# Kernel tuning notes

Hardware: AMD Instinct MI355X
Metric: run time of the kernel (lower is better)

Reference implementation:

```python
import jax, jax.numpy as jnp
import numpy as np

N, C, T, H, W = 4, 512, 8, 28, 28
CQ, CV = C // 8, C // 2  # 64, 256


def _maxpool222(a):
    # max_pool3d with kernel=stride=(2,2,2), VALID, over (t,h,w) of [n,c,t,h,w]
    return jax.lax.reduce_window(a, -jnp.inf, jax.lax.max,
                                 (1, 1, 2, 2, 2), (1, 1, 2, 2, 2), 'VALID')


def setup_inputs() -> dict:
    key = jax.random.key(0)
    ks = jax.random.split(key, 6)
    s = lambda fan_in: 1.0 / np.sqrt(fan_in)
    return {
        'x':  jax.random.normal(ks[0], (N, C, T, H, W), dtype=jnp.float32),
        'Wq': jax.random.normal(ks[1], (CQ, C), dtype=jnp.float32) * s(C),
        'Wk': jax.random.normal(ks[2], (CQ, C), dtype=jnp.float32) * s(C),
        'Wv': jax.random.normal(ks[3], (CV, C), dtype=jnp.float32) * s(C),
        'Wz': jax.random.normal(ks[4], (C, CV), dtype=jnp.float32) * s(CV),
        'y':  jax.random.normal(ks[5], (), dtype=jnp.float32) * 0.1,
    }


def reference(x, Wq, Wk, Wv, Wz, y):
    n, c, t, h, w = x.shape
    # 1x1x1 convs (no bias) = per-voxel channel mixing
    q = jnp.einsum('ncthw,oc->nothw', x, Wq)          # [n, CQ, t, h, w]
    k = _maxpool222(jnp.einsum('ncthw,oc->nothw', x, Wk))  # [n, CQ, t/2, h/2, w/2]
    v = _maxpool222(jnp.einsum('ncthw,oc->nothw', x, Wv))  # [n, CV, t/2, h/2, w/2]

    Lq = t * h * w
    Lk = k.shape[2] * k.shape[3] * k.shape[4]
    qf = q.reshape(n, q.shape[1], Lq)                 # [n, CQ, Lq]
    kf = k.reshape(n, k.shape[1], Lk)                 # [n, CQ, Lk]
    vf = v.reshape(n, v.shape[1], Lk)                 # [n, CV, Lk]

    # beta = softmax(q^T k) over kv axis (NOTE: no 1/sqrt(d) scaling, as in source)
    beta = jax.nn.softmax(jnp.einsum('ncq,nck->nqk', qf, kf), axis=-1)  # [n, Lq, Lk]
    att = jnp.einsum('nck,nqk->ncq', vf, beta)        # [n, CV, Lq]
    att = att.reshape(n, vf.shape[1], t, h, w)

    z = jnp.einsum('ncthw,oc->nothw', att, Wz)        # [n, C, t, h, w]
    return y * z + x
```

## Files before the change

### kernel.cpp

```cpp
#include <hip/hip_runtime.h>
#include <hip/hip_bf16.h>

#define LSP  6272
#define LK   784
#define CIN  512
#define CQo  64
#define CVo  256
#define NB   4

typedef __bf16  bf16x8 __attribute__((ext_vector_type(8)));
typedef __bf16  bf16x4 __attribute__((ext_vector_type(4)));
typedef float   f32x4  __attribute__((ext_vector_type(4)));

#define LDT  40

__global__ __launch_bounds__(256) void xt_kernel(const float* __restrict__ x,
                                                 __bf16* __restrict__ xT)
{
    __shared__ __attribute__((aligned(16))) __bf16 tile[64][68];
    int t = threadIdx.x;
    int p0 = blockIdx.x * 64, c0 = blockIdx.y * 64, n = blockIdx.z;
    #pragma unroll
    for (int i = 0; i < 4; i++) {
        int idx = i * 256 + t;
        int c = idx >> 4, p4 = (idx & 15) * 4;
        const float4 v = *reinterpret_cast<const float4*>(
            &x[((size_t)(n * CIN + c0 + c)) * LSP + p0 + p4]);
        tile[p4 + 0][c] = (__bf16)v.x;
        tile[p4 + 1][c] = (__bf16)v.y;
        tile[p4 + 2][c] = (__bf16)v.z;
        tile[p4 + 3][c] = (__bf16)v.w;
    }
    __syncthreads();
    #pragma unroll
    for (int i = 0; i < 4; i++) {
        int idx = i * 256 + t;
        int p = idx >> 4, c4 = (idx & 15) * 4;
        bf16x4 o;
        o[0] = tile[p][c4 + 0]; o[1] = tile[p][c4 + 1];
        o[2] = tile[p][c4 + 2]; o[3] = tile[p][c4 + 3];
        *reinterpret_cast<bf16x4*>(&xT[((size_t)(n * LSP + p0 + p)) * CIN + c0 + c4]) = o;
    }
}

__global__ void wprep_kernel(const float* __restrict__ Wq, const float* __restrict__ Wk,
                             const float* __restrict__ Wv, const float* __restrict__ Wz,
                             __bf16* __restrict__ Wqkv, __bf16* __restrict__ Wzb)
{
    int idx = blockIdx.x * 256 + threadIdx.x;
    if (idx < 384 * 512) {
        int o = idx >> 9;
        float v = (o < 64) ? Wq[idx] : (o < 128) ? Wk[idx - 64 * 512] : Wv[idx - 128 * 512];
        Wqkv[idx] = (__bf16)v;
    }
    if (idx < 512 * 256) Wzb[idx] = (__bf16)Wz[idx];
}

__global__ __launch_bounds__(256) void qkv_gemm(const __bf16* __restrict__ Wqkv,
                                                const __bf16* __restrict__ xT,
                                                __bf16* __restrict__ qT,
                                                __bf16* __restrict__ kT,
                                                __bf16* __restrict__ vconv)
{
    __shared__ __attribute__((aligned(16))) __bf16 As[2][128 * LDT];
    __shared__ __attribute__((aligned(16))) __bf16 Bs[2][128 * LDT];
    int t = threadIdx.x;
    int p0 = blockIdx.x * 128;
    int m0 = blockIdx.y * 128;
    int n  = blockIdx.z;
    int lane = t & 63, wid = t >> 6;
    int wm = wid >> 1, wn = wid & 1;
    int lm = lane & 15, lk = lane >> 4;

    const __bf16* wsrc = &Wqkv[(size_t)(m0 + (t >> 2)) * CIN + (t & 3) * 8];
    const __bf16* xsrc = &xT[((size_t)(n * LSP + p0 + (t >> 2))) * CIN + (t & 3) * 8];
    int dsoff = (t >> 2) * LDT + (t & 3) * 8;

    uint4 wa[2], xb[2];
    f32x4 acc[4][4] = {};

    wa[0] = *reinterpret_cast<const uint4*>(wsrc);
    wa[1] = *reinterpret_cast<const uint4*>(wsrc + 64 * CIN);
    xb[0] = *reinterpret_cast<const uint4*>(xsrc);
    xb[1] = *reinterpret_cast<const uint4*>(xsrc + 64 * CIN);
    *reinterpret_cast<uint4*>(&As[0][dsoff]) = wa[0];
    *reinterpret_cast<uint4*>(&As[0][dsoff + 64 * LDT]) = wa[1];
    *reinterpret_cast<uint4*>(&Bs[0][dsoff]) = xb[0];
    *reinterpret_cast<uint4*>(&Bs[0][dsoff + 64 * LDT]) = xb[1];
    __syncthreads();

    for (int kt = 0; kt < 16; kt++) {
        int cur = kt & 1;
        if (kt < 15) {
            int ko = (kt + 1) * 32;
            wa[0] = *reinterpret_cast<const uint4*>(wsrc + ko);
            wa[1] = *reinterpret_cast<const uint4*>(wsrc + 64 * CIN + ko);
            xb[0] = *reinterpret_cast<const uint4*>(xsrc + ko);
            xb[1] = *reinterpret_cast<const uint4*>(xsrc + 64 * CIN + ko);
        }
        bf16x8 a[4], b[4];
        if (m0 == 0) {
            #pragma unroll
            for (int mi = 0; mi < 4; mi++)
                a[mi] = *reinterpret_cast<const bf16x8*>(&As[cur][(wm * 64 + mi * 16 + lm) * LDT + lk * 8]);
            #pragma unroll
            for (int ni = 0; ni < 4; ni++)
                b[ni] = *reinterpret_cast<const bf16x8*>(&Bs[cur][(wn * 64 + ni * 16 + lm) * LDT + lk * 8]);
        } else {
            #pragma unroll
            for (int mi = 0; mi < 4; mi++)
                a[mi] = *reinterpret_cast<const bf16x8*>(&Bs[cur][(wn * 64 + mi * 16 + lm) * LDT + lk * 8]);
            #pragma unroll
            for (int ni = 0; ni < 4; ni++)
                b[ni] = *reinterpret_cast<const bf16x8*>(&As[cur][(wm * 64 + ni * 16 + lm) * LDT + lk * 8]);
        }
        #pragma unroll
        for (int mi = 0; mi < 4; mi++)
            #pragma unroll
            for (int ni = 0; ni < 4; ni++)
                acc[mi][ni] = __builtin_amdgcn_mfma_f32_16x16x32_bf16(a[mi], b[ni], acc[mi][ni], 0, 0, 0);
        if (kt < 15) {
            *reinterpret_cast<uint4*>(&As[cur ^ 1][dsoff]) = wa[0];
            *reinterpret_cast<uint4*>(&As[cur ^ 1][dsoff + 64 * LDT]) = wa[1];
            *reinterpret_cast<uint4*>(&Bs[cur ^ 1][dsoff]) = xb[0];
            *reinterpret_cast<uint4*>(&Bs[cur ^ 1][dsoff + 64 * LDT]) = xb[1];
        }
        __syncthreads();
    }

    if (m0 == 0) {
        #pragma unroll
        for (int mi = 0; mi < 4; mi++) {
            int mloc = wm * 64 + mi * 16 + lk * 4;
            #pragma unroll
            for (int ni = 0; ni < 4; ni++) {
                int p = p0 + wn * 64 + ni * 16 + lm;
                bf16x4 o;
                o[0] = (__bf16)acc[mi][ni][0]; o[1] = (__bf16)acc[mi][ni][1];
                o[2] = (__bf16)acc[mi][ni][2]; o[3] = (__bf16)acc[mi][ni][3];
                if (mloc < 64)
                    *reinterpret_cast<bf16x4*>(&qT[((size_t)(n * LSP + p)) * 64 + mloc]) = o;
                else
                    *reinterpret_cast<bf16x4*>(&kT[((size_t)(n * LSP + p)) * 64 + (mloc - 64)]) = o;
            }
        }
    } else {
        #pragma unroll
        for (int mi = 0; mi < 4; mi++) {
            int p = p0 + wn * 64 + mi * 16 + lk * 4;
            #pragma unroll
            for (int ni = 0; ni < 4; ni++) {
                int cv = (m0 - 128) + wm * 64 + ni * 16 + lm;
                bf16x4 o;
                o[0] = (__bf16)acc[mi][ni][0]; o[1] = (__bf16)acc[mi][ni][1];
                o[2] = (__bf16)acc[mi][ni][2]; o[3] = (__bf16)acc[mi][ni][3];
                *reinterpret_cast<bf16x4*>(&vconv[((size_t)(n * CVo + cv)) * LSP + p]) = o;
            }
        }
    }
}

__global__ __launch_bounds__(256) void poolk_kernel(const __bf16* __restrict__ kT,
                                                    __bf16* __restrict__ kpT)
{
    int wid = threadIdx.x >> 6, lane = threadIdx.x & 63;
    int row = blockIdx.x * 4 + wid;
    int n = row / LK, pk = row % LK;
    int tp = pk / 196, rem = pk % 196, hp = rem / 14, wp = rem % 14;
    const __bf16* b = kT + ((size_t)n * LSP + tp * 2 * 784 + hp * 2 * 28 + wp * 2) * 64 + lane;
    float m =        (float)b[0];
    m = fmaxf(m, (float)b[64]);
    m = fmaxf(m, (float)b[28 * 64]);
    m = fmaxf(m, (float)b[29 * 64]);
    m = fmaxf(m, (float)b[784 * 64]);
    m = fmaxf(m, (float)b[785 * 64]);
    m = fmaxf(m, (float)b[812 * 64]);
    m = fmaxf(m, (float)b[813 * 64]);
    kpT[(size_t)row * 64 + lane] = (__bf16)m;
}

__global__ void poolv_kernel(const __bf16* __restrict__ vconv, __bf16* __restrict__ vp)
{
    int id = blockIdx.x * 256 + threadIdx.x;
    if (id >= NB * CVo * LK) return;
    int nc = id / LK, pk = id % LK;
    int tp = pk / 196, rem = pk % 196, hp = rem / 14, wp = rem % 14;
    const __bf16* b = vconv + (size_t)nc * LSP + tp * 2 * 784 + hp * 2 * 28 + wp * 2;
    float m =        (float)b[0];
    m = fmaxf(m, (float)b[1]);   m = fmaxf(m, (float)b[28]);  m = fmaxf(m, (float)b[29]);
    m = fmaxf(m, (float)b[784]); m = fmaxf(m, (float)b[785]); m = fmaxf(m, (float)b[812]); m = fmaxf(m, (float)b[813]);
    vp[id] = (__bf16)m;
}

__global__ __launch_bounds__(512) void flash3_kernel(
    const __bf16* __restrict__ qT, const __bf16* __restrict__ kpT,
    const __bf16* __restrict__ vp, __bf16* __restrict__ attT)
{
    __shared__ __attribute__((aligned(16))) __bf16 Kbuf[2][64 * 64];
    __shared__ __attribute__((aligned(16))) __bf16 Ps[128 * 64];
    __shared__ float scs[128];
    __shared__ float invl[128];

    int t = threadIdx.x;
    int lane = t & 63, w = t >> 6;
    int lm = lane & 15, lk = lane >> 4;
    int q0 = blockIdx.x * 128;
    int n  = blockIdx.y;
    int swz = (lm & 7) << 3;

    const __bf16* kbase = kpT + (size_t)n * LK * 64;
    const __bf16* vbase = vp  + (size_t)n * CVo * LK;

    bf16x8 qa[2];
    {
        const __bf16* qrow = &qT[((size_t)(n * LSP + q0 + w * 16 + lm)) * 64 + lk * 8];
        qa[0] = *reinterpret_cast<const bf16x8*>(qrow);
        qa[1] = *reinterpret_cast<const bf16x8*>(qrow + 32);
    }

    int kr = t >> 3, kc = t & 7;
    int kds = kr * 64 + ((kc * 8) ^ ((kr & 7) << 3));
    const __bf16* kgsrc = &kbase[(size_t)kr * 64 + kc * 8];

    const __bf16* vsrc[2][2];
    #pragma unroll
    for (int mi = 0; mi < 2; mi++)
        #pragma unroll
        for (int ks = 0; ks < 2; ks++)
            vsrc[mi][ks] = &vbase[(size_t)(w * 32 + mi * 16 + lm) * LK + ks * 32 + lk * 8];

    uint4 kreg;
    bf16x8 vcur[2][2], vnxt[2][2];

    kreg = *reinterpret_cast<const uint4*>(kgsrc);
    #pragma unroll
    for (int mi = 0; mi < 2; mi++)
        #pragma unroll
        for (int ks = 0; ks < 2; ks++)
            vcur[mi][ks] = *reinterpret_cast<const bf16x8*>(vsrc[mi][ks]);
    *reinterpret_cast<uint4*>(&Kbuf[0][kds]) = kreg;
    __syncthreads();

    f32x4 accO[2][8] = {};
    float m = -1e30f, l = 0.0f;
    int qrow = w * 16 + lm;

    for (int kt = 0; kt < 13; kt++) {
        int cur = kt & 1;
        bool have_next = (kt < 12);
        bool lastT = (kt == 12);
        if (have_next) {
            size_t off = (size_t)(kt + 1) * 64;
            kreg = *reinterpret_cast<const uint4*>(kgsrc + off * 64);
            #pragma unroll
            for (int mi = 0; mi < 2; mi++)
                #pragma unroll
                for (int ks = 0; ks < 2; ks++)
                    vnxt[mi][ks] = *reinterpret_cast<const bf16x8*>(vsrc[mi][ks] + off);
        }
        f32x4 accS[4] = {};
        #pragma unroll
        for (int kg = 0; kg < 4; kg++) {
            if (!lastT || kg == 0) {
                #pragma unroll
                for (int ks = 0; ks < 2; ks++) {
                    bf16x8 kf = *reinterpret_cast<const bf16x8*>(
                        &Kbuf[cur][(kg * 16 + lm) * 64 + ((ks * 32 + lk * 8) ^ swz)]);
                    accS[kg] = __builtin_amdgcn_mfma_f32_16x16x32_bf16(kf, qa[ks], accS[kg], 0, 0, 0);
                }
            } else {
                accS[kg][0] = -1e30f; accS[kg][1] = -1e30f;
                accS[kg][2] = -1e30f; accS[kg][3] = -1e30f;
            }
        }
        float v = -1e30f;
        #pragma unroll
        for (int kg = 0; kg < 4; kg++)
            #pragma unroll
            for (int r = 0; r < 4; r++) v = fmaxf(v, accS[kg][r]);
        v = fmaxf(v, __shfl_xor(v, 16));
        v = fmaxf(v, __shfl_xor(v, 32));
        float sc_out = 1.0f;
        if (__any(v - m > 8.0f)) {
            float mn = fmaxf(m, v);
            sc_out = __expf(m - mn);
            l *= sc_out;
            m = mn;
        }
        float lt = 0.0f;
        #pragma unroll
        for (int kg = 0; kg < 4; kg++) {
            bf16x4 pw;
            #pragma unroll
            for (int r = 0; r < 4; r++) {
                float p = __expf(accS[kg][r] - m);
                lt += p;
                pw[r] = (__bf16)p;
            }
            *reinterpret_cast<bf16x4*>(&Ps[qrow * 64 + ((kg * 16 + lk * 4) ^ swz)]) = pw;
        }
        lt += __shfl_xor(lt, 16);
        lt += __shfl_xor(lt, 32);
        l += lt;
        if (lk == 0) scs[qrow] = sc_out;
        __syncthreads();
        float s[8];
        #pragma unroll
        for (int ni = 0; ni < 8; ni++) s[ni] = scs[ni * 16 + lm];
        bool need = false;
        #pragma unroll
        for (int ni = 0; ni < 8; ni++) need = need || (s[ni] != 1.0f);
        if (__any(need)) {
            #pragma unroll
            for (int mi = 0; mi < 2; mi++)
                #pragma unroll
                for (int ni = 0; ni < 8; ni++)
                    #pragma unroll
                    for (int r = 0; r < 4; r++) accO[mi][ni][r] *= s[ni];
        }
        #pragma unroll
        for (int ks = 0; ks < 2; ks++) {
            bf16x8 pf[8];
            #pragma unroll
            for (int ni = 0; ni < 8; ni++)
                pf[ni] = *reinterpret_cast<const bf16x8*>(
                    &Ps[(ni * 16 + lm) * 64 + ((ks * 32 + lk * 8) ^ swz)]);
            #pragma unroll
            for (int mi = 0; mi < 2; mi++)
                #pragma unroll
                for (int ni = 0; ni < 8; ni++)
                    accO[mi][ni] = __builtin_amdgcn_mfma_f32_16x16x32_bf16(
                        vcur[mi][ks], pf[ni], accO[mi][ni], 0, 0, 0);
        }
        if (have_next)
            *reinterpret_cast<uint4*>(&Kbuf[cur ^ 1][kds]) = kreg;
        __syncthreads();
        #pragma unroll
        for (int mi = 0; mi < 2; mi++)
            #pragma unroll
            for (int ks = 0; ks < 2; ks++)
                vcur[mi][ks] = vnxt[mi][ks];
    }
    if (lk == 0) invl[qrow] = 1.0f / l;
    __syncthreads();
    #pragma unroll
    for (int ni = 0; ni < 8; ni++) {
        float inv = invl[ni * 16 + lm];
        __bf16* orow = &attT[((size_t)(n * LSP + q0 + ni * 16 + lm)) * CVo + w * 32 + lk * 4];
        #pragma unroll
        for (int mi = 0; mi < 2; mi++) {
            bf16x4 o;
            o[0] = (__bf16)(accO[mi][ni][0] * inv);
            o[1] = (__bf16)(accO[mi][ni][1] * inv);
            o[2] = (__bf16)(accO[mi][ni][2] * inv);
            o[3] = (__bf16)(accO[mi][ni][3] * inv);
            *reinterpret_cast<bf16x4*>(&orow[mi * 16]) = o;
        }
    }
}

__global__ __launch_bounds__(256) void z_gemm(const __bf16* __restrict__ Wzb,
                                              const __bf16* __restrict__ attT,
                                              const float* __restrict__ x,
                                              const float* __restrict__ yp,
                                              float* __restrict__ out)
{
    __shared__ __attribute__((aligned(16))) __bf16 As[2][128 * LDT];
    __shared__ __attribute__((aligned(16))) __bf16 Bs[2][128 * LDT];
    int t = threadIdx.x;
    int p0 = blockIdx.x * 128;
    int c0 = blockIdx.y * 128;
    int n  = blockIdx.z;
    int lane = t & 63, wid = t >> 6;
    int wm = wid >> 1, wn = wid & 1;
    int lm = lane & 15, lk = lane >> 4;

    const __bf16* asrc = &attT[((size_t)(n * LSP + p0 + (t >> 2))) * CVo + (t & 3) * 8];
    const __bf16* bsrc = &Wzb[(size_t)(c0 + (t >> 2)) * CVo + (t & 3) * 8];
    int dsoff = (t >> 2) * LDT + (t & 3) * 8;

    uint4 aa[2], bb[2];
    f32x4 acc[4][4] = {};

    aa[0] = *reinterpret_cast<const uint4*>(asrc);
    aa[1] = *reinterpret_cast<const uint4*>(asrc + 64 * CVo);
    bb[0] = *reinterpret_cast<const uint4*>(bsrc);
    bb[1] = *reinterpret_cast<const uint4*>(bsrc + 64 * CVo);
    *reinterpret_cast<uint4*>(&As[0][dsoff]) = aa[0];
    *reinterpret_cast<uint4*>(&As[0][dsoff + 64 * LDT]) = aa[1];
    *reinterpret_cast<uint4*>(&Bs[0][dsoff]) = bb[0];
    *reinterpret_cast<uint4*>(&Bs[0][dsoff + 64 * LDT]) = bb[1];
    __syncthreads();

    for (int kt = 0; kt < 8; kt++) {
        int cur = kt & 1;
        if (kt < 7) {
            int ko = (kt + 1) * 32;
            aa[0] = *reinterpret_cast<const uint4*>(asrc + ko);
            aa[1] = *reinterpret_cast<const uint4*>(asrc + 64 * CVo + ko);
            bb[0] = *reinterpret_cast<const uint4*>(bsrc + ko);
            bb[1] = *reinterpret_cast<const uint4*>(bsrc + 64 * CVo + ko);
        }
        bf16x8 a[4], b[4];
        #pragma unroll
        for (int mi = 0; mi < 4; mi++)
            a[mi] = *reinterpret_cast<const bf16x8*>(&As[cur][(wm * 64 + mi * 16 + lm) * LDT + lk * 8]);
        #pragma unroll
        for (int ni = 0; ni < 4; ni++)
            b[ni] = *reinterpret_cast<const bf16x8*>(&Bs[cur][(wn * 64 + ni * 16 + lm) * LDT + lk * 8]);
        #pragma unroll
        for (int mi = 0; mi < 4; mi++)
            #pragma unroll
            for (int ni = 0; ni < 4; ni++)
                acc[mi][ni] = __builtin_amdgcn_mfma_f32_16x16x32_bf16(a[mi], b[ni], acc[mi][ni], 0, 0, 0);
        if (kt < 7) {
            *reinterpret_cast<uint4*>(&As[cur ^ 1][dsoff]) = aa[0];
            *reinterpret_cast<uint4*>(&As[cur ^ 1][dsoff + 64 * LDT]) = aa[1];
            *reinterpret_cast<uint4*>(&Bs[cur ^ 1][dsoff]) = bb[0];
            *reinterpret_cast<uint4*>(&Bs[cur ^ 1][dsoff + 64 * LDT]) = bb[1];
        }
        __syncthreads();
    }

    float yv = yp[0];
    #pragma unroll
    for (int mi = 0; mi < 4; mi++) {
        int p = p0 + wm * 64 + mi * 16 + lk * 4;
        #pragma unroll
        for (int ni = 0; ni < 4; ni++) {
            int c = c0 + wn * 64 + ni * 16 + lm;
            size_t o = ((size_t)(n * CIN + c)) * LSP + p;
            const float4 xv = *reinterpret_cast<const float4*>(&x[o]);
            float4 ov;
            ov.x = yv * acc[mi][ni][0] + xv.x;
            ov.y = yv * acc[mi][ni][1] + xv.y;
            ov.z = yv * acc[mi][ni][2] + xv.z;
            ov.w = yv * acc[mi][ni][3] + xv.w;
            *reinterpret_cast<float4*>(&out[o]) = ov;
        }
    }
}

extern "C" void kernel_launch(void* const* d_in, const int* in_sizes, int n_in,
                              void* d_out, int out_size, void* d_ws, size_t ws_size,
                              hipStream_t stream)
{
    const float* x  = (const float*)d_in[0];
    const float* Wq = (const float*)d_in[1];
    const float* Wk = (const float*)d_in[2];
    const float* Wv = (const float*)d_in[3];
    const float* Wz = (const float*)d_in[4];
    const float* y  = (const float*)d_in[5];
    float* out = (float*)d_out;
    __bf16* ws = (__bf16*)d_ws;

    __bf16* xT    = ws;
    __bf16* kT    = ws + (size_t)12845056;
    __bf16* vconv = ws + (size_t)14450688;
    __bf16* qT    = ws + (size_t)20873216;
    __bf16* kpT   = ws + (size_t)22478848;
    __bf16* vp    = ws + (size_t)22679552;
    __bf16* attT  = ws + (size_t)23482368;
    __bf16* Wqkv  = ws + (size_t)29904896;
    __bf16* Wzb   = ws + (size_t)30101504;

    xt_kernel     <<<dim3(98, 8, 4), 256, 0, stream>>>(x, xT);
    wprep_kernel  <<<dim3(768), 256, 0, stream>>>(Wq, Wk, Wv, Wz, Wqkv, Wzb);
    qkv_gemm      <<<dim3(49, 3, 4), 256, 0, stream>>>(Wqkv, xT, qT, kT, vconv);
    poolk_kernel  <<<dim3(784), 256, 0, stream>>>(kT, kpT);
    poolv_kernel  <<<dim3(3136), 256, 0, stream>>>(vconv, vp);
    flash3_kernel <<<dim3(49, 4), 512, 0, stream>>>(qT, kpT, vp, attT);
    z_gemm        <<<dim3(49, 4, 4), 256, 0, stream>>>(Wzb, attT, x, y, out);
}
```

Baseline: 210.8 us.

## Halve spatial tile in qkv and z GEMMs, swizzle block order, single-buffer z_gemm

Both 1x1-conv GEMMs now use 64-voxel spatial tiles instead of 128, doubling the grid (1176 and 1568 blocks) so the 256 CUs are better filled and each block holds fewer accumulators. A linear-to-swizzled block index remaps tiles so consecutive blocks are spread across XCDs, aiming for better L2 locality of shared x and weight tiles. z_gemm drops LDS double-buffering for a single buffer with two barriers per k-step, cutting LDS use to raise occupancy. The trade is more redundant weight loads and more barrier stalls per k-step.

```diff
diff --git a/kernel.cpp b/kernel.cpp
--- a/kernel.cpp
+++ b/kernel.cpp
@@ -63,30 +63,30 @@
                                                 __bf16* __restrict__ vconv)
 {
     __shared__ __attribute__((aligned(16))) __bf16 As[2][128 * LDT];
-    __shared__ __attribute__((aligned(16))) __bf16 Bs[2][128 * LDT];
+    __shared__ __attribute__((aligned(16))) __bf16 Bs[2][64 * LDT];
     int t = threadIdx.x;
-    int p0 = blockIdx.x * 128;
-    int m0 = blockIdx.y * 128;
-    int n  = blockIdx.z;
+    int lin = blockIdx.x + 3 * blockIdx.y + 294 * blockIdx.z;
+    int swz = (lin & 7) * 147 + (lin >> 3);
+    int n = swz / 294, rr = swz % 294;
+    int pt = rr / 3, mt = rr % 3;
+    int p0 = pt * 64, m0 = mt * 128;
     int lane = t & 63, wid = t >> 6;
     int wm = wid >> 1, wn = wid & 1;
     int lm = lane & 15, lk = lane >> 4;
 
     const __bf16* wsrc = &Wqkv[(size_t)(m0 + (t >> 2)) * CIN + (t & 3) * 8];
     const __bf16* xsrc = &xT[((size_t)(n * LSP + p0 + (t >> 2))) * CIN + (t & 3) * 8];
-    int dsoff = (t >> 2) * LDT + (t & 3) * 8;
-
-    uint4 wa[2], xb[2];
-    f32x4 acc[4][4] = {};
+    int dso = (t >> 2) * LDT + (t & 3) * 8;
+
+    uint4 wa[2], xb;
+    f32x4 accF[8] = {};
 
     wa[0] = *reinterpret_cast<const uint4*>(wsrc);
     wa[1] = *reinterpret_cast<const uint4*>(wsrc + 64 * CIN);
-    xb[0] = *reinterpret_cast<const uint4*>(xsrc);
-    xb[1] = *reinterpret_cast<const uint4*>(xsrc + 64 * CIN);
-    *reinterpret_cast<uint4*>(&As[0][dsoff]) = wa[0];
-    *reinterpret_cast<uint4*>(&As[0][dsoff + 64 * LDT]) = wa[1];
-    *reinterpret_cast<uint4*>(&Bs[0][dsoff]) = xb[0];
-    *reinterpret_cast<uint4*>(&Bs[0][dsoff + 64 * LDT]) = xb[1];
+    xb    = *reinterpret_cast<const uint4*>(xsrc);
+    *reinterpret_cast<uint4*>(&As[0][dso]) = wa[0];
+    *reinterpret_cast<uint4*>(&As[0][dso + 64 * LDT]) = wa[1];
+    *reinterpret_cast<uint4*>(&Bs[0][dso]) = xb;
     __syncthreads();
 
     for (int kt = 0; kt < 16; kt++) {
@@ -95,35 +95,39 @@
             int ko = (kt + 1) * 32;
             wa[0] = *reinterpret_cast<const uint4*>(wsrc + ko);
             wa[1] = *reinterpret_cast<const uint4*>(wsrc + 64 * CIN + ko);
-            xb[0] = *reinterpret_cast<const uint4*>(xsrc + ko);
-            xb[1] = *reinterpret_cast<const uint4*>(xsrc + 64 * CIN + ko);
-        }
-        bf16x8 a[4], b[4];
+            xb    = *reinterpret_cast<const uint4*>(xsrc + ko);
+        }
         if (m0 == 0) {
+            bf16x8 a[4], b[2];
             #pragma unroll
             for (int mi = 0; mi < 4; mi++)
                 a[mi] = *reinterpret_cast<const bf16x8*>(&As[cur][(wm * 64 + mi * 16 + lm) * LDT + lk * 8]);
             #pragma unroll
-            for (int ni = 0; ni < 4; ni++)
-                b[ni] = *reinterpret_cast<const bf16x8*>(&Bs[cur][(wn * 64 + ni * 16 + lm) * LDT + lk * 8]);
+            for (int ni = 0; ni < 2; ni++)
+                b[ni] = *reinterpret_cast<const bf16x8*>(&Bs[cur][(wn * 32 + ni * 16 + lm) * LDT + lk * 8]);
+            #pragma unroll
+            for (int mi = 0; mi < 4; mi++)
+                #pragma unroll
+                for (int ni = 0; ni < 2; ni++)
+                    accF[mi * 2 + ni] = __builtin_amdgcn_mfma_f32_16x16x32_bf16(a[mi], b[ni], accF[mi * 2 + ni], 0, 0, 0);
         } else {
-            #pragma unroll
-            for (int mi = 0; mi < 4; mi++)
-                a[mi] = *reinterpret_cast<const bf16x8*>(&Bs[cur][(wn * 64 + mi * 16 + lm) * LDT + lk * 8]);
+            bf16x8 a[2], b[4];
+            #pragma unroll
+            for (int mi = 0; mi < 2; mi++)
+                a[mi] = *reinterpret_cast<const bf16x8*>(&Bs[cur][(wn * 32 + mi * 16 + lm) * LDT + lk * 8]);
             #pragma unroll
             for (int ni = 0; ni < 4; ni++)
                 b[ni] = *reinterpret_cast<const bf16x8*>(&As[cur][(wm * 64 + ni * 16 + lm) * LDT + lk * 8]);
-        }
-        #pragma unroll
-        for (int mi = 0; mi < 4; mi++)
-            #pragma unroll
-            for (int ni = 0; ni < 4; ni++)
-                acc[mi][ni] = __builtin_amdgcn_mfma_f32_16x16x32_bf16(a[mi], b[ni], acc[mi][ni], 0, 0, 0);
+            #pragma unroll
+            for (int mi = 0; mi < 2; mi++)
+                #pragma unroll
+                for (int ni = 0; ni < 4; ni++)
+                    accF[mi * 4 + ni] = __builtin_amdgcn_mfma_f32_16x16x32_bf16(a[mi], b[ni], accF[mi * 4 + ni], 0, 0, 0);
+        }
         if (kt < 15) {
-            *reinterpret_cast<uint4*>(&As[cur ^ 1][dsoff]) = wa[0];
-            *reinterpret_cast<uint4*>(&As[cur ^ 1][dsoff + 64 * LDT]) = wa[1];
-            *reinterpret_cast<uint4*>(&Bs[cur ^ 1][dsoff]) = xb[0];
-            *reinterpret_cast<uint4*>(&Bs[cur ^ 1][dsoff + 64 * LDT]) = xb[1];
+            *reinterpret_cast<uint4*>(&As[cur ^ 1][dso]) = wa[0];
+            *reinterpret_cast<uint4*>(&As[cur ^ 1][dso + 64 * LDT]) = wa[1];
+            *reinterpret_cast<uint4*>(&Bs[cur ^ 1][dso]) = xb;
         }
         __syncthreads();
     }
@@ -133,11 +137,12 @@
         for (int mi = 0; mi < 4; mi++) {
             int mloc = wm * 64 + mi * 16 + lk * 4;
             #pragma unroll
-            for (int ni = 0; ni < 4; ni++) {
-                int p = p0 + wn * 64 + ni * 16 + lm;
+            for (int ni = 0; ni < 2; ni++) {
+                int p = p0 + wn * 32 + ni * 16 + lm;
+                f32x4 ac = accF[mi * 2 + ni];
                 bf16x4 o;
-                o[0] = (__bf16)acc[mi][ni][0]; o[1] = (__bf16)acc[mi][ni][1];
-                o[2] = (__bf16)acc[mi][ni][2]; o[3] = (__bf16)acc[mi][ni][3];
+                o[0] = (__bf16)ac[0]; o[1] = (__bf16)ac[1];
+                o[2] = (__bf16)ac[2]; o[3] = (__bf16)ac[3];
                 if (mloc < 64)
                     *reinterpret_cast<bf16x4*>(&qT[((size_t)(n * LSP + p)) * 64 + mloc]) = o;
                 else
@@ -146,14 +151,15 @@
         }
     } else {
         #pragma unroll
-        for (int mi = 0; mi < 4; mi++) {
-            int p = p0 + wn * 64 + mi * 16 + lk * 4;
+        for (int mi = 0; mi < 2; mi++) {
+            int p = p0 + wn * 32 + mi * 16 + lk * 4;
             #pragma unroll
             for (int ni = 0; ni < 4; ni++) {
                 int cv = (m0 - 128) + wm * 64 + ni * 16 + lm;
+                f32x4 ac = accF[mi * 4 + ni];
                 bf16x4 o;
-                o[0] = (__bf16)acc[mi][ni][0]; o[1] = (__bf16)acc[mi][ni][1];
-                o[2] = (__bf16)acc[mi][ni][2]; o[3] = (__bf16)acc[mi][ni][3];
+                o[0] = (__bf16)ac[0]; o[1] = (__bf16)ac[1];
+                o[2] = (__bf16)ac[2]; o[3] = (__bf16)ac[3];
                 *reinterpret_cast<bf16x4*>(&vconv[((size_t)(n * CVo + cv)) * LSP + p]) = o;
             }
         }
@@ -365,77 +371,75 @@
                                               const float* __restrict__ yp,
                                               float* __restrict__ out)
 {
-    __shared__ __attribute__((aligned(16))) __bf16 As[2][128 * LDT];
-    __shared__ __attribute__((aligned(16))) __bf16 Bs[2][128 * LDT];
+    __shared__ __attribute__((aligned(16))) __bf16 As[64 * LDT];
+    __shared__ __attribute__((aligned(16))) __bf16 Bs[128 * LDT];
     int t = threadIdx.x;
-    int p0 = blockIdx.x * 128;
-    int c0 = blockIdx.y * 128;
-    int n  = blockIdx.z;
+    int lin = blockIdx.x + 4 * blockIdx.y + 392 * blockIdx.z;
+    int swz = (lin & 7) * 196 + (lin >> 3);
+    int n = swz / 392, rr = swz % 392;
+    int pt = rr / 4, ct = rr % 4;
+    int p0 = pt * 64, c0 = ct * 128;
     int lane = t & 63, wid = t >> 6;
-    int wm = wid >> 1, wn = wid & 1;
+    int wp = wid & 1, wc = wid >> 1;
     int lm = lane & 15, lk = lane >> 4;
 
     const __bf16* asrc = &attT[((size_t)(n * LSP + p0 + (t >> 2))) * CVo + (t & 3) * 8];
     const __bf16* bsrc = &Wzb[(size_t)(c0 + (t >> 2)) * CVo + (t & 3) * 8];
-    int dsoff = (t >> 2) * LDT + (t & 3) * 8;
-
-    uint4 aa[2], bb[2];
-    f32x4 acc[4][4] = {};
-
-    aa[0] = *reinterpret_cast<const uint4*>(asrc);
-    aa[1] = *reinterpret_cast<const uint4*>(asrc + 64 * CVo);
+    int dso = (t >> 2) * LDT + (t & 3) * 8;
+
+    uint4 aa, bb[2];
+    f32x4 acc[2][4] = {};
+
+    aa    = *reinterpret_cast<const uint4*>(asrc);
     bb[0] = *reinterpret_cast<const uint4*>(bsrc);
     bb[1] = *reinterpret_cast<const uint4*>(bsrc + 64 * CVo);
-    *reinterpret_cast<uint4*>(&As[0][dsoff]) = aa[0];
-    *reinterpret_cast<uint4*>(&As[0][dsoff + 64 * LDT]) = aa[1];
-    *reinterpret_cast<uint4*>(&Bs[0][dsoff]) = bb[0];
-    *reinterpret_cast<uint4*>(&Bs[0][dsoff + 64 * LDT]) = bb[1];
+    *reinterpret_cast<uint4*>(&As[dso]) = aa;
+    *reinterpret_cast<uint4*>(&Bs[dso]) = bb[0];
+    *reinterpret_cast<uint4*>(&Bs[dso + 64 * LDT]) = bb[1];
     __syncthreads();
 
     for (int kt = 0; kt < 8; kt++) {
-        int cur = kt & 1;
         if (kt < 7) {
             int ko = (kt + 1) * 32;
-            aa[0] = *reinterpret_cast<const uint4*>(asrc + ko);
-            aa[1] = *reinterpret_cast<const uint4*>(asrc + 64 * CVo + ko);
+            aa    = *reinterpret_cast<const uint4*>(asrc + ko);
             bb[0] = *reinterpret_cast<const uint4*>(bsrc + ko);
             bb[1] = *reinterpret_cast<const uint4*>(bsrc + 64 * CVo + ko);
         }
-        bf16x8 a[4], b[4];
-        #pragma unroll
-        for (int mi = 0; mi < 4; mi++)
-            a[mi] = *reinterpret_cast<const bf16x8*>(&As[cur][(wm * 64 + mi * 16 + lm) * LDT + lk * 8]);
-        #pragma unroll
-        for (int ni = 0; ni < 4; ni++)
-            b[ni] = *reinterpret_cast<const bf16x8*>(&Bs[cur][(wn * 64 + ni * 16 + lm) * LDT + lk * 8]);
-        #pragma unroll
-        for (int mi = 0; mi < 4; mi++)
-            #pragma unroll
-            for (int ni = 0; ni < 4; ni++)
-                acc[mi][ni] = __builtin_amdgcn_mfma_f32_16x16x32_bf16(a[mi], b[ni], acc[mi][ni], 0, 0, 0);
+        bf16x8 a[2], b[4];
+        #pragma unroll
+        for (int ai = 0; ai < 2; ai++)
+            a[ai] = *reinterpret_cast<const bf16x8*>(&As[(wp * 32 + ai * 16 + lm) * LDT + lk * 8]);
+        #pragma unroll
+        for (int bi = 0; bi < 4; bi++)
+            b[bi] = *reinterpret_cast<const bf16x8*>(&Bs[(wc * 64 + bi * 16 + lm) * LDT + lk * 8]);
+        #pragma unroll
+        for (int ai = 0; ai < 2; ai++)
+            #pragma unroll
+            for (int bi = 0; bi < 4; bi++)
+                acc[ai][bi] = __builtin_amdgcn_mfma_f32_16x16x32_bf16(a[ai], b[bi], acc[ai][bi], 0, 0, 0);
         if (kt < 7) {
-            *reinterpret_cast<uint4*>(&As[cur ^ 1][dsoff]) = aa[0];
-            *reinterpret_cast<uint4*>(&As[cur ^ 1][dsoff + 64 * LDT]) = aa[1];
-            *reinterpret_cast<uint4*>(&Bs[cur ^ 1][dsoff]) = bb[0];
-            *reinterpret_cast<uint4*>(&Bs[cur ^ 1][dsoff + 64 * LDT]) = bb[1];
-        }
-        __syncthreads();
+            __syncthreads();
+            *reinterpret_cast<uint4*>(&As[dso]) = aa;
+            *reinterpret_cast<uint4*>(&Bs[dso]) = bb[0];
+            *reinterpret_cast<uint4*>(&Bs[dso + 64 * LDT]) = bb[1];
+            __syncthreads();
+        }
     }
 
     float yv = yp[0];
     #pragma unroll
-    for (int mi = 0; mi < 4; mi++) {
-        int p = p0 + wm * 64 + mi * 16 + lk * 4;
-        #pragma unroll
-        for (int ni = 0; ni < 4; ni++) {
-            int c = c0 + wn * 64 + ni * 16 + lm;
+    for (int ai = 0; ai < 2; ai++) {
+        int p = p0 + wp * 32 + ai * 16 + lk * 4;
+        #pragma unroll
+        for (int bi = 0; bi < 4; bi++) {
+            int c = c0 + wc * 64 + bi * 16 + lm;
             size_t o = ((size_t)(n * CIN + c)) * LSP + p;
             const float4 xv = *reinterpret_cast<const float4*>(&x[o]);
             float4 ov;
-            ov.x = yv * acc[mi][ni][0] + xv.x;
-            ov.y = yv * acc[mi][ni][1] + xv.y;
-            ov.z = yv * acc[mi][ni][2] + xv.z;
-            ov.w = yv * acc[mi][ni][3] + xv.w;
+            ov.x = yv * acc[ai][bi][0] + xv.x;
+            ov.y = yv * acc[ai][bi][1] + xv.y;
+            ov.z = yv * acc[ai][bi][2] + xv.z;
+            ov.w = yv * acc[ai][bi][3] + xv.w;
             *reinterpret_cast<float4*>(&out[o]) = ov;
         }
     }
@@ -466,9 +470,9 @@
 
     xt_kernel     <<<dim3(98, 8, 4), 256, 0, stream>>>(x, xT);
     wprep_kernel  <<<dim3(768), 256, 0, stream>>>(Wq, Wk, Wv, Wz, Wqkv, Wzb);
-    qkv_gemm      <<<dim3(49, 3, 4), 256, 0, stream>>>(Wqkv, xT, qT, kT, vconv);
+    qkv_gemm      <<<dim3(3, 98, 4), 256, 0, stream>>>(Wqkv, xT, qT, kT, vconv);
     poolk_kernel  <<<dim3(784), 256, 0, stream>>>(kT, kpT);
     poolv_kernel  <<<dim3(3136), 256, 0, stream>>>(vconv, vp);
     flash3_kernel <<<dim3(49, 4), 512, 0, stream>>>(qT, kpT, vp, attT);
-    z_gemm        <<<dim3(49, 4, 4), 256, 0, stream>>>(Wzb, attT, x, y, out);
-}
+    z_gemm        <<<dim3(4, 98, 4), 256, 0, stream>>>(Wzb, attT, x, y, out);
+}
```

After: 216.0 us. 1.03x slower.
